# Kernel optimization log

Hardware: AMD Instinct MI355X
Metric: run time of the kernel (lower is better)

Reference implementation:

```python
import jax, jax.numpy as jnp
import numpy as np

DIM = 768
HEADS = 12
HEAD_DIM = DIM // HEADS  # 64
SCALE = HEAD_DIM ** -0.5
B, H, W = 16, 64, 64
EPS_BN = 1e-5
EPS_SQRT = 1e-5


def setup_inputs() -> dict:
    key = jax.random.key(0)
    k0, k1, k2, k3, k4 = jax.random.split(key, 5)
    x = jax.random.normal(k0, (B, DIM, H, W), dtype=jnp.float32)
    # 1x1 conv == pointwise matmul over channels
    qkv_w = jax.random.normal(k1, (3 * DIM, DIM), dtype=jnp.float32) * (DIM ** -0.5)
    qkv_b = jax.random.normal(k2, (3 * DIM,), dtype=jnp.float32) * 0.01
    gamma = 1.0 + 0.1 * jax.random.normal(k3, (DIM,), dtype=jnp.float32)
    beta = 0.1 * jax.random.normal(k4, (DIM,), dtype=jnp.float32)
    return {"x": x, "qkv_w": qkv_w, "qkv_b": qkv_b, "gamma": gamma, "beta": beta}


def reference(x, qkv_w, qkv_b, gamma, beta):
    b, c, h, w = x.shape
    n = h * w
    xf = x.reshape(b, c, n)  # [B, C, N]
    # qkv 1x1 conv
    qkv = jnp.einsum('oc,bcn->bon', qkv_w, xf) + qkv_b[None, :, None]  # [B, 3C, N]
    qkv = qkv.reshape(b, 3, HEADS, HEAD_DIM, n)
    q, k, v = qkv[:, 0], qkv[:, 1], qkv[:, 2]  # each [B, h, d, N]
    # channel attention: contract over N -> [B, h, d, d]
    attn = jnp.einsum('bhdn,bhen->bhde', q, k) * SCALE
    attn = jnp.sign(attn) * jnp.sqrt(jnp.abs(attn) + EPS_SQRT)
    attn = jax.nn.softmax(attn, axis=-1)
    # BatchNorm2d (training-mode batch statistics, biased variance) + ReLU
    mean = jnp.mean(x, axis=(0, 2, 3))
    var = jnp.var(x, axis=(0, 2, 3))
    y = (x - mean[None, :, None, None]) * jax.lax.rsqrt(var + EPS_BN)[None, :, None, None]
    y = y * gamma[None, :, None, None] + beta[None, :, None, None]
    out = jnp.maximum(y, 0.0)
    # original module discards attn; returned here so the attention math is
    return out, attn
```

## Files before the change

### kernel.cpp

```cpp
#include <hip/hip_runtime.h>
#include <hip/hip_bf16.h>

#define DIM 768
#define NB 16
#define NPOS 4096
#define HEADS 12

typedef unsigned short u16;
typedef __attribute__((ext_vector_type(4))) float f32x4;
typedef __attribute__((ext_vector_type(8))) short s16x8;
typedef __attribute__((ext_vector_type(4))) u16 u16x4;

static __device__ __forceinline__ u16 f2bf(float f) {
  __hip_bfloat16 h = __float2bfloat16(f);
  u16 u; __builtin_memcpy(&u, &h, 2); return u;
}

static __device__ __forceinline__ void load_lds16(const void* g, void* l) {
  __builtin_amdgcn_global_load_lds(
      (const __attribute__((address_space(1))) unsigned int*)g,
      (__attribute__((address_space(3))) unsigned int*)l, 16, 0, 0);
}

static __device__ __forceinline__ int lds_idx(int row, int slotf) {
  return row * 64 + (((slotf) ^ (row & 7)) << 3);
}


__global__ __launch_bounds__(128) void sums_cast_kernel(const float* __restrict__ x,
                                                        float* __restrict__ sum_bc,
                                                        float* __restrict__ sumsq_bc,
                                                        u16* __restrict__ Xb) {
  int bc = blockIdx.x;
  const float4* p = (const float4*)(x + (size_t)bc * NPOS);
  u16x4* ob = (u16x4*)(Xb + (size_t)bc * NPOS);
  int t = threadIdx.x;
  float s = 0.f, ss = 0.f;
  for (int i = t; i < NPOS / 4; i += 128) {
    float4 v = p[i];
    s  += v.x + v.y + v.z + v.w;
    ss += v.x * v.x + v.y * v.y + v.z * v.z + v.w * v.w;
    u16x4 hv = {f2bf(v.x), f2bf(v.y), f2bf(v.z), f2bf(v.w)};
    ob[i] = hv;
  }
  for (int off = 32; off; off >>= 1) { s += __shfl_down(s, off); ss += __shfl_down(ss, off); }
  __shared__ float red[4];
  int lane = t & 63, w = t >> 6;
  if (lane == 0) { red[w] = s; red[2 + w] = ss; }
  __syncthreads();
  if (t == 0) { sum_bc[bc] = red[0] + red[1]; sumsq_bc[bc] = red[2] + red[3]; }
}

__global__ void finalize_kernel(const float* __restrict__ sum_bc, const float* __restrict__ sumsq_bc,
                                const float* __restrict__ gamma, const float* __restrict__ beta,
                                float* __restrict__ chanScale, float* __restrict__ chanShift) {
  int c = blockIdx.x * blockDim.x + threadIdx.x;
  if (c >= DIM) return;
  float s = 0.f, ss = 0.f;
  for (int b = 0; b < NB; b++) { s += sum_bc[b * DIM + c]; ss += sumsq_bc[b * DIM + c]; }
  const float invn = 1.f / ((float)NB * (float)NPOS);
  float mean = s * invn;
  float var  = ss * invn - mean * mean;
  float rstd = rsqrtf(var + 1e-5f);
  float a = rstd * gamma[c];
  chanScale[c] = a;
  chanShift[c] = beta[c] - mean * a;
}

__global__ __launch_bounds__(256) void bn_kernel(const float* __restrict__ x,
                                                 const float* __restrict__ chanScale,
                                                 const float* __restrict__ chanShift,
                                                 float* __restrict__ out) {
  const size_t n4 = (size_t)NB * DIM * NPOS / 4;
  const float4* x4 = (const float4*)x;
  float4* o4 = (float4*)out;
  for (size_t i = (size_t)blockIdx.x * blockDim.x + threadIdx.x; i < n4;
       i += (size_t)gridDim.x * blockDim.x) {
    float4 v = x4[i];
    int c = (int)((i >> 10) % DIM);
    float a = chanScale[c], sh = chanShift[c];
    v.x = fmaxf(fmaf(v.x, a, sh), 0.f);
    v.y = fmaxf(fmaf(v.y, a, sh), 0.f);
    v.z = fmaxf(fmaf(v.z, a, sh), 0.f);
    v.w = fmaxf(fmaf(v.w, a, sh), 0.f);
    o4[i] = v;
  }
}


__global__ __launch_bounds__(64) void tvecw_kernel(const float* __restrict__ W,
                                                   const float* __restrict__ sum_bc,
                                                   float* __restrict__ tvec,
                                                   u16* __restrict__ Wb) {
  int r = blockIdx.x;
  int lane = threadIdx.x;
  const float* wr = W + (size_t)r * DIM;
  float acc[NB];
#pragma unroll
  for (int b = 0; b < NB; b++) acc[b] = 0.f;
#pragma unroll
  for (int j = 0; j < DIM / 64; j++) {
    int c = lane + j * 64;
    float wv = wr[c];
    Wb[(size_t)r * DIM + c] = f2bf(wv);
#pragma unroll
    for (int b = 0; b < NB; b++) acc[b] += wv * sum_bc[b * DIM + c];
  }
#pragma unroll
  for (int b = 0; b < NB; b++) {
    float v = acc[b];
    for (int off = 32; off; off >>= 1) v += __shfl_down(v, off);
    if (lane == 0) tvec[(size_t)b * 1536 + r] = v;
  }
}


template <bool SYMM>
__global__ __launch_bounds__(256) void gemm_kernel(
    const u16* __restrict__ A, long long strideA,
    const u16* __restrict__ B, long long strideB,
    u16* __restrict__ C, long long strideC,
    int lda, int ldb, int ldc, int K) {
  __shared__ __align__(16) u16 As[128 * 64];
  __shared__ __align__(16) u16 Bs[128 * 64];

  int ti, tj, bz;
  if (SYMM) {
    bz = blockIdx.y;
    int idx = blockIdx.x, rem = 6;
    ti = 0;
    while (idx >= rem) { idx -= rem; ti++; rem--; }
    tj = ti + idx;
  } else {
    ti = blockIdx.x; tj = blockIdx.y; bz = blockIdx.z;
  }
  const u16* Ab = A + (size_t)bz * strideA;
  const u16* Bb = B + (size_t)bz * strideB;
  u16* Cb = C + (size_t)bz * strideC;
  int ib = ti * 128, jb = tj * 128;

  int t = threadIdx.x, lane = t & 63, w = t >> 6;
  int wr = (w >> 1) * 64, wc = (w & 1) * 64;
  int fr = lane & 15, q4 = lane >> 4;
  int srow = lane >> 3;
  int sslot = (lane & 7) ^ srow;

  f32x4 acc[4][4];
#pragma unroll
  for (int m = 0; m < 4; m++)
#pragma unroll
    for (int n = 0; n < 4; n++) acc[m][n] = (f32x4){0.f, 0.f, 0.f, 0.f};

  for (int k0 = 0; k0 < K; k0 += 64) {
#pragma unroll
    for (int i = 0; i < 4; i++) {
      int q = w * 4 + i;
      int row = q * 8 + srow;
      load_lds16(Ab + (size_t)(ib + row) * lda + k0 + sslot * 8, (char*)As + q * 1024);
      load_lds16(Bb + (size_t)(jb + row) * ldb + k0 + sslot * 8, (char*)Bs + q * 1024);
    }
    __syncthreads();
#pragma unroll
    for (int kk = 0; kk < 2; kk++) {
      int sbase = kk * 4 + q4;
      s16x8 af[4], bfv[4];
#pragma unroll
      for (int m = 0; m < 4; m++) af[m] = *(const s16x8*)&As[lds_idx(wr + m * 16 + fr, sbase)];
#pragma unroll
      for (int n = 0; n < 4; n++) bfv[n] = *(const s16x8*)&Bs[lds_idx(wc + n * 16 + fr, sbase)];
#pragma unroll
      for (int m = 0; m < 4; m++)
#pragma unroll
        for (int n = 0; n < 4; n++)
          acc[m][n] = __builtin_amdgcn_mfma_f32_16x16x32_bf16(af[m], bfv[n], acc[m][n], 0, 0, 0);
    }
    __syncthreads();
  }

  int rbase = q4 * 4;
#pragma unroll
  for (int m = 0; m < 4; m++)
#pragma unroll
    for (int n = 0; n < 4; n++)
#pragma unroll
      for (int r = 0; r < 4; r++) {
        int row = ib + wr + m * 16 + rbase + r;
        int col = jb + wc + n * 16 + fr;
        u16 v = f2bf(acc[m][n][r]);
        Cb[(size_t)row * ldc + col] = v;
        if (SYMM && ti != tj) Cb[(size_t)col * ldc + row] = v;
      }
}


__global__ __launch_bounds__(256) void attn_kernel(const u16* __restrict__ Pb,
                                                   const u16* __restrict__ Wb,
                                                   const float* __restrict__ bias,
                                                   const float* __restrict__ tvec,
                                                   float* __restrict__ outAttn) {
  int h = blockIdx.x, b = blockIdx.y;
  __shared__ __align__(16) u16 As[64 * 64];
  __shared__ __align__(16) u16 Bs[64 * 64];
  __shared__ float sm[64 * 65];
  const u16* Pa = Pb + ((size_t)b * DIM + h * 64) * DIM;
  const u16* Wk = Wb + (size_t)(DIM + h * 64) * DIM;

  int t = threadIdx.x, lane = t & 63, w = t >> 6;
  int fr = lane & 15, q4 = lane >> 4;
  int srow = lane >> 3;
  int sslot = (lane & 7) ^ srow;

  f32x4 acc[4];
#pragma unroll
  for (int n = 0; n < 4; n++) acc[n] = (f32x4){0.f, 0.f, 0.f, 0.f};

  for (int k0 = 0; k0 < DIM; k0 += 64) {
#pragma unroll
    for (int i = 0; i < 2; i++) {
      int q = w * 2 + i;
      int row = q * 8 + srow;
      load_lds16(Pa + (size_t)row * DIM + k0 + sslot * 8, (char*)As + q * 1024);
      load_lds16(Wk + (size_t)row * DIM + k0 + sslot * 8, (char*)Bs + q * 1024);
    }
    __syncthreads();
#pragma unroll
    for (int kk = 0; kk < 2; kk++) {
      int sbase = kk * 4 + q4;
      s16x8 af = *(const s16x8*)&As[lds_idx(w * 16 + fr, sbase)];
#pragma unroll
      for (int n = 0; n < 4; n++) {
        s16x8 bfv = *(const s16x8*)&Bs[lds_idx(n * 16 + fr, sbase)];
        acc[n] = __builtin_amdgcn_mfma_f32_16x16x32_bf16(af, bfv, acc[n], 0, 0, 0);
      }
    }
    __syncthreads();
  }

  const float* tq = tvec + (size_t)b * 1536 + h * 64;
  const float* tk = tq + DIM;
  const float* bq = bias + h * 64;
  const float* bk = bias + DIM + h * 64;
  int rbase = q4 * 4;
#pragma unroll
  for (int n = 0; n < 4; n++) {
    int e = n * 16 + fr;
    float bke = bk[e], tke = tk[e];
#pragma unroll
    for (int r = 0; r < 4; r++) {
      int d = w * 16 + rbase + r;
      float bqd = bq[d];
      float raw = acc[n][r] + bqd * tke + bke * tq[d] + 4096.f * bqd * bke;
      float val = 0.125f * raw;
      float sq = sqrtf(fabsf(val) + 1e-5f);
      sm[d * 65 + e] = val > 0.f ? sq : (val < 0.f ? -sq : 0.f);
    }
  }
  __syncthreads();
  if (t < 64) {
    int d = t;
    float mx = -1e30f;
    for (int e2 = 0; e2 < 64; e2++) mx = fmaxf(mx, sm[d * 65 + e2]);
    float s = 0.f;
    for (int e2 = 0; e2 < 64; e2++) s += __expf(sm[d * 65 + e2] - mx);
    float inv = 1.f / s;
    float* o = outAttn + (((size_t)b * HEADS + h) * 64 + d) * 64;
    for (int e2 = 0; e2 < 64; e2++) o[e2] = __expf(sm[d * 65 + e2] - mx) * inv;
  }
}


extern "C" void kernel_launch(void* const* d_in, const int* in_sizes, int n_in,
                              void* d_out, int out_size, void* d_ws, size_t ws_size,
                              hipStream_t stream) {
  const float* x     = (const float*)d_in[0];
  const float* qkv_w = (const float*)d_in[1];
  const float* qkv_b = (const float*)d_in[2];
  const float* gamma = (const float*)d_in[3];
  const float* beta  = (const float*)d_in[4];
  float* out = (float*)d_out;
  float* ws  = (float*)d_ws;

  float* sum_bc    = ws;
  float* sumsq_bc  = ws + 12288;
  float* chanScale = ws + 24576;
  float* chanShift = ws + 25344;
  float* tvec      = ws + 26112;
  u16* Wb = (u16*)(ws + 50688);
  u16* Gb = (u16*)((char*)d_ws + 2562048);
  u16* Pb = (u16*)((char*)d_ws + 2562048 + 18874368);

  u16* Xb = (u16*)d_out;

  sums_cast_kernel<<<NB * DIM, 128, 0, stream>>>(x, sum_bc, sumsq_bc, Xb);
  finalize_kernel<<<3, 256, 0, stream>>>(sum_bc, sumsq_bc, gamma, beta, chanScale, chanShift);
  tvecw_kernel<<<2 * DIM, 64, 0, stream>>>(qkv_w, sum_bc, tvec, Wb);
  gemm_kernel<true><<<dim3(21, NB), 256, 0, stream>>>(
      Xb, (long long)DIM * NPOS, Xb, (long long)DIM * NPOS, Gb, (long long)DIM * DIM,
      NPOS, NPOS, DIM, NPOS);
  bn_kernel<<<2048, 256, 0, stream>>>(x, chanScale, chanShift, out);
  gemm_kernel<false><<<dim3(6, 6, NB), 256, 0, stream>>>(
      Wb, 0LL, Gb, (long long)DIM * DIM, Pb, (long long)DIM * DIM,
      DIM, DIM, DIM, DIM);
  attn_kernel<<<dim3(HEADS, NB), 256, 0, stream>>>(Pb, Wb, qkv_b, tvec,
                                                   out + (size_t)NB * DIM * NPOS);
}
```

Baseline: 313.6 us.

## Split-K the symmetric Gram GEMM with fp32 partials and parallelize softmax

```diff
diff --git a/kernel.cpp b/kernel.cpp
--- a/kernel.cpp
+++ b/kernel.cpp
@@ -115,7 +115,90 @@
 }
 
 
-template <bool SYMM>
+__global__ __launch_bounds__(256) void gram_kernel(const u16* __restrict__ X,
+                                                   float* __restrict__ Gpart) {
+  __shared__ __align__(16) u16 As[128 * 64];
+  __shared__ __align__(16) u16 Bs[128 * 64];
+  int bz = blockIdx.y;
+  int s = blockIdx.x & 1;
+  int idx = blockIdx.x >> 1, rem = 6, ti = 0;
+  while (idx >= rem) { idx -= rem; ti++; rem--; }
+  int tj = ti + idx;
+  const u16* Xb = X + (size_t)bz * DIM * NPOS;
+  int ib = ti * 128, jb = tj * 128;
+  int kbeg = s * 2048;
+
+  int t = threadIdx.x, lane = t & 63, w = t >> 6;
+  int wr = (w >> 1) * 64, wc = (w & 1) * 64;
+  int fr = lane & 15, q4 = lane >> 4;
+  int srow = lane >> 3;
+  int sslot = (lane & 7) ^ srow;
+
+  f32x4 acc[4][4];
+#pragma unroll
+  for (int m = 0; m < 4; m++)
+#pragma unroll
+    for (int n = 0; n < 4; n++) acc[m][n] = (f32x4){0.f, 0.f, 0.f, 0.f};
+
+  for (int k0 = kbeg; k0 < kbeg + 2048; k0 += 64) {
+#pragma unroll
+    for (int i = 0; i < 4; i++) {
+      int q = w * 4 + i;
+      int row = q * 8 + srow;
+      load_lds16(Xb + (size_t)(ib + row) * NPOS + k0 + sslot * 8, (char*)As + q * 1024);
+      load_lds16(Xb + (size_t)(jb + row) * NPOS + k0 + sslot * 8, (char*)Bs + q * 1024);
+    }
+    __syncthreads();
+#pragma unroll
+    for (int kk = 0; kk < 2; kk++) {
+      int sbase = kk * 4 + q4;
+      s16x8 af[4], bfv[4];
+#pragma unroll
+      for (int m = 0; m < 4; m++) af[m] = *(const s16x8*)&As[lds_idx(wr + m * 16 + fr, sbase)];
+#pragma unroll
+      for (int n = 0; n < 4; n++) bfv[n] = *(const s16x8*)&Bs[lds_idx(wc + n * 16 + fr, sbase)];
+#pragma unroll
+      for (int m = 0; m < 4; m++)
+#pragma unroll
+        for (int n = 0; n < 4; n++)
+          acc[m][n] = __builtin_amdgcn_mfma_f32_16x16x32_bf16(af[m], bfv[n], acc[m][n], 0, 0, 0);
+    }
+    __syncthreads();
+  }
+
+  float* Cp = Gpart + (size_t)s * (NB * DIM * DIM) + (size_t)bz * DIM * DIM;
+  int rbase = q4 * 4;
+#pragma unroll
+  for (int m = 0; m < 4; m++)
+#pragma unroll
+    for (int n = 0; n < 4; n++)
+#pragma unroll
+      for (int r = 0; r < 4; r++) {
+        int row = ib + wr + m * 16 + rbase + r;
+        int col = jb + wc + n * 16 + fr;
+        float v = acc[m][n][r];
+        Cp[(size_t)row * DIM + col] = v;
+        if (ti != tj) Cp[(size_t)col * DIM + row] = v;
+      }
+}
+
+__global__ __launch_bounds__(256) void reduce_kernel(const float* __restrict__ G0,
+                                                     const float* __restrict__ G1,
+                                                     u16* __restrict__ Gb) {
+  const size_t n4 = (size_t)NB * DIM * DIM / 4;
+  const f32x4* a = (const f32x4*)G0;
+  const f32x4* c = (const f32x4*)G1;
+  u16x4* o = (u16x4*)Gb;
+  for (size_t i = (size_t)blockIdx.x * 256 + threadIdx.x; i < n4;
+       i += (size_t)gridDim.x * 256) {
+    f32x4 va = a[i], vc = c[i];
+    u16x4 hv = {f2bf(va[0] + vc[0]), f2bf(va[1] + vc[1]),
+                f2bf(va[2] + vc[2]), f2bf(va[3] + vc[3])};
+    o[i] = hv;
+  }
+}
+
+
 __global__ __launch_bounds__(256) void gemm_kernel(
     const u16* __restrict__ A, long long strideA,
     const u16* __restrict__ B, long long strideB,
@@ -123,17 +206,7 @@
     int lda, int ldb, int ldc, int K) {
   __shared__ __align__(16) u16 As[128 * 64];
   __shared__ __align__(16) u16 Bs[128 * 64];
-
-  int ti, tj, bz;
-  if (SYMM) {
-    bz = blockIdx.y;
-    int idx = blockIdx.x, rem = 6;
-    ti = 0;
-    while (idx >= rem) { idx -= rem; ti++; rem--; }
-    tj = ti + idx;
-  } else {
-    ti = blockIdx.x; tj = blockIdx.y; bz = blockIdx.z;
-  }
+  int ti = blockIdx.x, tj = blockIdx.y, bz = blockIdx.z;
   const u16* Ab = A + (size_t)bz * strideA;
   const u16* Bb = B + (size_t)bz * strideB;
   u16* Cb = C + (size_t)bz * strideC;
@@ -186,9 +259,7 @@
       for (int r = 0; r < 4; r++) {
         int row = ib + wr + m * 16 + rbase + r;
         int col = jb + wc + n * 16 + fr;
-        u16 v = f2bf(acc[m][n][r]);
-        Cb[(size_t)row * ldc + col] = v;
-        if (SYMM && ti != tj) Cb[(size_t)col * ldc + row] = v;
+        Cb[(size_t)row * ldc + col] = f2bf(acc[m][n][r]);
       }
 }
 
@@ -256,15 +327,23 @@
     }
   }
   __syncthreads();
-  if (t < 64) {
-    int d = t;
+  {
+    int d = t >> 2, qd = (t & 3) * 16;
+    const float* row = &sm[d * 65];
     float mx = -1e30f;
-    for (int e2 = 0; e2 < 64; e2++) mx = fmaxf(mx, sm[d * 65 + e2]);
-    float s = 0.f;
-    for (int e2 = 0; e2 < 64; e2++) s += __expf(sm[d * 65 + e2] - mx);
-    float inv = 1.f / s;
+#pragma unroll
+    for (int e2 = 0; e2 < 16; e2++) mx = fmaxf(mx, row[qd + e2]);
+    mx = fmaxf(mx, __shfl_xor(mx, 1));
+    mx = fmaxf(mx, __shfl_xor(mx, 2));
+    float sum = 0.f;
+#pragma unroll
+    for (int e2 = 0; e2 < 16; e2++) sum += __expf(row[qd + e2] - mx);
+    sum += __shfl_xor(sum, 1);
+    sum += __shfl_xor(sum, 2);
+    float inv = 1.f / sum;
     float* o = outAttn + (((size_t)b * HEADS + h) * 64 + d) * 64;
-    for (int e2 = 0; e2 < 64; e2++) o[e2] = __expf(sm[d * 65 + e2] - mx) * inv;
+#pragma unroll
+    for (int e2 = 0; e2 < 16; e2++) o[qd + e2] = __expf(row[qd + e2] - mx) * inv;
   }
 }
 
@@ -290,15 +369,16 @@
   u16* Pb = (u16*)((char*)d_ws + 2562048 + 18874368);
 
   u16* Xb = (u16*)d_out;
+  float* G0 = (float*)((char*)d_out + 100663296);
+  float* G1 = G0 + (size_t)NB * DIM * DIM;
 
   sums_cast_kernel<<<NB * DIM, 128, 0, stream>>>(x, sum_bc, sumsq_bc, Xb);
   finalize_kernel<<<3, 256, 0, stream>>>(sum_bc, sumsq_bc, gamma, beta, chanScale, chanShift);
   tvecw_kernel<<<2 * DIM, 64, 0, stream>>>(qkv_w, sum_bc, tvec, Wb);
-  gemm_kernel<true><<<dim3(21, NB), 256, 0, stream>>>(
-      Xb, (long long)DIM * NPOS, Xb, (long long)DIM * NPOS, Gb, (long long)DIM * DIM,
-      NPOS, NPOS, DIM, NPOS);
+  gram_kernel<<<dim3(42, NB), 256, 0, stream>>>(Xb, G0);
+  reduce_kernel<<<2048, 256, 0, stream>>>(G0, G1, Gb);
   bn_kernel<<<2048, 256, 0, stream>>>(x, chanScale, chanShift, out);
-  gemm_kernel<false><<<dim3(6, 6, NB), 256, 0, stream>>>(
+  gemm_kernel<<<dim3(6, 6, NB), 256, 0, stream>>>(
       Wb, 0LL, Gb, (long long)DIM * DIM, Pb, (long long)DIM * DIM,
       DIM, DIM, DIM, DIM);
   attn_kernel<<<dim3(HEADS, NB), 256, 0, stream>>>(Pb, Wb, qkv_b, tvec,
```

Result: slower. 329.8 us (+5.2%).

## Double-buffer LDS in GEMM and attention kernels, swizzle blocks, parallelize softmax

Applied to the files above, without the earlier changes.

```diff
diff --git a/kernel.cpp b/kernel.cpp
--- a/kernel.cpp
+++ b/kernel.cpp
@@ -121,13 +121,15 @@
     const u16* __restrict__ B, long long strideB,
     u16* __restrict__ C, long long strideC,
     int lda, int ldb, int ldc, int K) {
-  __shared__ __align__(16) u16 As[128 * 64];
-  __shared__ __align__(16) u16 Bs[128 * 64];
+  __shared__ __align__(16) u16 As[2][128 * 64];
+  __shared__ __align__(16) u16 Bs[2][128 * 64];
 
   int ti, tj, bz;
   if (SYMM) {
-    bz = blockIdx.y;
-    int idx = blockIdx.x, rem = 6;
+    int bid = blockIdx.x;
+    int swz = (bid & 7) * 42 + (bid >> 3);
+    bz = swz / 21;
+    int idx = swz % 21, rem = 6;
     ti = 0;
     while (idx >= rem) { idx -= rem; ti++; rem--; }
     tj = ti + idx;
@@ -145,37 +147,55 @@
   int srow = lane >> 3;
   int sslot = (lane & 7) ^ srow;
 
+  const u16* Asrc = Ab + (size_t)ib * lda + (size_t)srow * lda + sslot * 8;
+  const u16* Bsrc = Bb + (size_t)jb * ldb + (size_t)srow * ldb + sslot * 8;
+
   f32x4 acc[4][4];
 #pragma unroll
   for (int m = 0; m < 4; m++)
 #pragma unroll
     for (int n = 0; n < 4; n++) acc[m][n] = (f32x4){0.f, 0.f, 0.f, 0.f};
 
-  for (int k0 = 0; k0 < K; k0 += 64) {
-#pragma unroll
-    for (int i = 0; i < 4; i++) {
-      int q = w * 4 + i;
-      int row = q * 8 + srow;
-      load_lds16(Ab + (size_t)(ib + row) * lda + k0 + sslot * 8, (char*)As + q * 1024);
-      load_lds16(Bb + (size_t)(jb + row) * ldb + k0 + sslot * 8, (char*)Bs + q * 1024);
-    }
+#define STAGE(buf, k0)                                                          \
+  {                                                                             \
+    _Pragma("unroll")                                                           \
+    for (int i = 0; i < 4; i++) {                                               \
+      int q = w * 4 + i;                                                        \
+      load_lds16(Asrc + (size_t)(q * 8) * lda + (k0), (char*)As[buf] + q * 1024);\
+      load_lds16(Bsrc + (size_t)(q * 8) * ldb + (k0), (char*)Bs[buf] + q * 1024);\
+    }                                                                           \
+  }
+
+#define COMPUTE(buf)                                                            \
+  {                                                                             \
+    _Pragma("unroll")                                                           \
+    for (int kk = 0; kk < 2; kk++) {                                            \
+      int sbase = kk * 4 + q4;                                                  \
+      s16x8 af[4], bfv[4];                                                      \
+      _Pragma("unroll")                                                         \
+      for (int m = 0; m < 4; m++) af[m] = *(const s16x8*)&As[buf][lds_idx(wr + m * 16 + fr, sbase)]; \
+      _Pragma("unroll")                                                         \
+      for (int n = 0; n < 4; n++) bfv[n] = *(const s16x8*)&Bs[buf][lds_idx(wc + n * 16 + fr, sbase)]; \
+      _Pragma("unroll")                                                         \
+      for (int m = 0; m < 4; m++)                                               \
+        _Pragma("unroll")                                                       \
+        for (int n = 0; n < 4; n++)                                             \
+          acc[m][n] = __builtin_amdgcn_mfma_f32_16x16x32_bf16(af[m], bfv[n], acc[m][n], 0, 0, 0); \
+    }                                                                           \
+  }
+
+  STAGE(0, 0);
+  __syncthreads();
+  for (int k0 = 0; k0 < K; k0 += 128) {
+    STAGE(1, k0 + 64);
+    COMPUTE(0);
     __syncthreads();
-#pragma unroll
-    for (int kk = 0; kk < 2; kk++) {
-      int sbase = kk * 4 + q4;
-      s16x8 af[4], bfv[4];
-#pragma unroll
-      for (int m = 0; m < 4; m++) af[m] = *(const s16x8*)&As[lds_idx(wr + m * 16 + fr, sbase)];
-#pragma unroll
-      for (int n = 0; n < 4; n++) bfv[n] = *(const s16x8*)&Bs[lds_idx(wc + n * 16 + fr, sbase)];
-#pragma unroll
-      for (int m = 0; m < 4; m++)
-#pragma unroll
-        for (int n = 0; n < 4; n++)
-          acc[m][n] = __builtin_amdgcn_mfma_f32_16x16x32_bf16(af[m], bfv[n], acc[m][n], 0, 0, 0);
-    }
+    if (k0 + 128 < K) STAGE(0, k0 + 128);
+    COMPUTE(1);
     __syncthreads();
   }
+#undef STAGE
+#undef COMPUTE
 
   int rbase = q4 * 4;
 #pragma unroll
@@ -199,8 +219,8 @@
                                                    const float* __restrict__ tvec,
                                                    float* __restrict__ outAttn) {
   int h = blockIdx.x, b = blockIdx.y;
-  __shared__ __align__(16) u16 As[64 * 64];
-  __shared__ __align__(16) u16 Bs[64 * 64];
+  __shared__ __align__(16) u16 As[2][64 * 64];
+  __shared__ __align__(16) u16 Bs[2][64 * 64];
   __shared__ float sm[64 * 65];
   const u16* Pa = Pb + ((size_t)b * DIM + h * 64) * DIM;
   const u16* Wk = Wb + (size_t)(DIM + h * 64) * DIM;
@@ -210,31 +230,49 @@
   int srow = lane >> 3;
   int sslot = (lane & 7) ^ srow;
 
+  const u16* Asrc = Pa + (size_t)srow * DIM + sslot * 8;
+  const u16* Bsrc = Wk + (size_t)srow * DIM + sslot * 8;
+
   f32x4 acc[4];
 #pragma unroll
   for (int n = 0; n < 4; n++) acc[n] = (f32x4){0.f, 0.f, 0.f, 0.f};
 
-  for (int k0 = 0; k0 < DIM; k0 += 64) {
-#pragma unroll
-    for (int i = 0; i < 2; i++) {
-      int q = w * 2 + i;
-      int row = q * 8 + srow;
-      load_lds16(Pa + (size_t)row * DIM + k0 + sslot * 8, (char*)As + q * 1024);
-      load_lds16(Wk + (size_t)row * DIM + k0 + sslot * 8, (char*)Bs + q * 1024);
-    }
+#define ASTAGE(buf, k0)                                                         \
+  {                                                                             \
+    _Pragma("unroll")                                                           \
+    for (int i = 0; i < 2; i++) {                                               \
+      int q = w * 2 + i;                                                        \
+      load_lds16(Asrc + (size_t)(q * 8) * DIM + (k0), (char*)As[buf] + q * 1024);\
+      load_lds16(Bsrc + (size_t)(q * 8) * DIM + (k0), (char*)Bs[buf] + q * 1024);\
+    }                                                                           \
+  }
+
+#define ACOMPUTE(buf)                                                           \
+  {                                                                             \
+    _Pragma("unroll")                                                           \
+    for (int kk = 0; kk < 2; kk++) {                                            \
+      int sbase = kk * 4 + q4;                                                  \
+      s16x8 af = *(const s16x8*)&As[buf][lds_idx(w * 16 + fr, sbase)];          \
+      _Pragma("unroll")                                                         \
+      for (int n = 0; n < 4; n++) {                                             \
+        s16x8 bfv = *(const s16x8*)&Bs[buf][lds_idx(n * 16 + fr, sbase)];       \
+        acc[n] = __builtin_amdgcn_mfma_f32_16x16x32_bf16(af, bfv, acc[n], 0, 0, 0); \
+      }                                                                         \
+    }                                                                           \
+  }
+
+  ASTAGE(0, 0);
+  __syncthreads();
+  for (int k0 = 0; k0 < DIM; k0 += 128) {
+    ASTAGE(1, k0 + 64);
+    ACOMPUTE(0);
     __syncthreads();
-#pragma unroll
-    for (int kk = 0; kk < 2; kk++) {
-      int sbase = kk * 4 + q4;
-      s16x8 af = *(const s16x8*)&As[lds_idx(w * 16 + fr, sbase)];
-#pragma unroll
-      for (int n = 0; n < 4; n++) {
-        s16x8 bfv = *(const s16x8*)&Bs[lds_idx(n * 16 + fr, sbase)];
-        acc[n] = __builtin_amdgcn_mfma_f32_16x16x32_bf16(af, bfv, acc[n], 0, 0, 0);
-      }
-    }
+    if (k0 + 128 < DIM) ASTAGE(0, k0 + 128);
+    ACOMPUTE(1);
     __syncthreads();
   }
+#undef ASTAGE
+#undef ACOMPUTE
 
   const float* tq = tvec + (size_t)b * 1536 + h * 64;
   const float* tk = tq + DIM;
@@ -256,15 +294,23 @@
     }
   }
   __syncthreads();
-  if (t < 64) {
-    int d = t;
+  {
+    int d = t >> 2, qd = (t & 3) * 16;
+    const float* row = &sm[d * 65];
     float mx = -1e30f;
-    for (int e2 = 0; e2 < 64; e2++) mx = fmaxf(mx, sm[d * 65 + e2]);
-    float s = 0.f;
-    for (int e2 = 0; e2 < 64; e2++) s += __expf(sm[d * 65 + e2] - mx);
-    float inv = 1.f / s;
+#pragma unroll
+    for (int e2 = 0; e2 < 16; e2++) mx = fmaxf(mx, row[qd + e2]);
+    mx = fmaxf(mx, __shfl_xor(mx, 1));
+    mx = fmaxf(mx, __shfl_xor(mx, 2));
+    float sum = 0.f;
+#pragma unroll
+    for (int e2 = 0; e2 < 16; e2++) sum += __expf(row[qd + e2] - mx);
+    sum += __shfl_xor(sum, 1);
+    sum += __shfl_xor(sum, 2);
+    float inv = 1.f / sum;
     float* o = outAttn + (((size_t)b * HEADS + h) * 64 + d) * 64;
-    for (int e2 = 0; e2 < 64; e2++) o[e2] = __expf(sm[d * 65 + e2] - mx) * inv;
+#pragma unroll
+    for (int e2 = 0; e2 < 16; e2++) o[qd + e2] = __expf(row[qd + e2] - mx) * inv;
   }
 }
 
@@ -294,7 +340,7 @@
   sums_cast_kernel<<<NB * DIM, 128, 0, stream>>>(x, sum_bc, sumsq_bc, Xb);
   finalize_kernel<<<3, 256, 0, stream>>>(sum_bc, sumsq_bc, gamma, beta, chanScale, chanShift);
   tvecw_kernel<<<2 * DIM, 64, 0, stream>>>(qkv_w, sum_bc, tvec, Wb);
-  gemm_kernel<true><<<dim3(21, NB), 256, 0, stream>>>(
+  gemm_kernel<true><<<336, 256, 0, stream>>>(
       Xb, (long long)DIM * NPOS, Xb, (long long)DIM * NPOS, Gb, (long long)DIM * DIM,
       NPOS, NPOS, DIM, NPOS);
   bn_kernel<<<2048, 256, 0, stream>>>(x, chanScale, chanShift, out);
```

New measurement: 320.2 us. 1.02x slower.
